# Kernel tuning notes

Hardware: AMD Instinct MI355X
Metric: run time of the kernel (lower is better)

Reference implementation:

```python
import jax, jax.numpy as jnp
import numpy as np

BN_EPS = 1e-5


def _bn_relu(h, gamma, beta):
    # BatchNorm1d in training mode: batch stats over the edge dimension, biased var
    mu = jnp.mean(h, axis=0)
    var = jnp.mean((h - mu) ** 2, axis=0)
    return jax.nn.relu((h - mu) * jax.lax.rsqrt(var + BN_EPS) * gamma + beta)


def setup_inputs() -> dict:
    key = jax.random.key(0)
    ks = jax.random.split(key, 6)
    B, P, C, O, K = 8, 2048, 64, 64, 20  # clouds, points/cloud, in_ch, out_ch, knn
    N = B * P
    x = jax.random.normal(ks[0], (N, C), jnp.float32)
    pos = jax.random.normal(ks[1], (N, 3), jnp.float32)
    batch = jnp.repeat(jnp.arange(B, dtype=jnp.int32), P)  # sorted cloud ids
    # MLP params: Linear(2C, O) -> BN -> ReLU -> Linear(O, O) -> BN -> ReLU
    W1 = jax.random.normal(ks[2], (O, 2 * C), jnp.float32) / np.sqrt(2 * C)
    b1 = jnp.zeros((O,), jnp.float32)
    g1 = jnp.ones((O,), jnp.float32)
    beta1 = jnp.zeros((O,), jnp.float32)
    W2 = jax.random.normal(ks[3], (O, O), jnp.float32) / np.sqrt(O)
    b2 = jnp.zeros((O,), jnp.float32)
    g2 = jnp.ones((O,), jnp.float32)
    beta2 = jnp.zeros((O,), jnp.float32)
    return {"x": x, "pos": pos, "batch": batch, "W1": W1, "b1": b1, "g1": g1,
            "beta1": beta1, "W2": W2, "b2": b2, "g2": g2, "beta2": beta2, "k": K}


def reference(x, pos, batch, W1, b1, g1, beta1, W2, b2, g2, beta2, k):
    N, C = x.shape
    B = int(batch[-1]) + 1          # equal-size, sorted clouds
    P = N // B
    p = pos.reshape(B, P, -1)
    # knn_graph (loop=False): brute-force squared distances per cloud
    sq = jnp.sum(p * p, axis=-1)                      # [B,P]
    d2 = sq[:, :, None] + sq[:, None, :] - 2.0 * jnp.einsum('bpd,bqd->bpq', p, p)
    d2 = jnp.where(jnp.eye(P, dtype=bool)[None], jnp.inf, d2)  # no self-loops
    _, nbr = jax.lax.top_k(-d2, k)                    # [B,P,k] neighbor idx in cloud
    offset = (jnp.arange(B, dtype=nbr.dtype) * P)[:, None, None]
    # torch_cluster knn_graph flow='source_to_target': row = neighbor j, col = center i
    row = (nbr + offset).reshape(-1)                  # [N*k]
    col = jnp.repeat(jnp.arange(N, dtype=row.dtype), k)
    x_r = x[row]
    edge_features = jnp.concatenate([x_r, x[col] - x_r], axis=1)  # [N*k, 2C]
    h = _bn_relu(edge_features @ W1.T + b1, g1, beta1)
    h = _bn_relu(h @ W2.T + b2, g2, beta2)
    out = jax.ops.segment_max(h, row, num_segments=N)
    # torch_scatter scatter(reduce='max') leaves empty rows at 0
    return jnp.where(jnp.isneginf(out), 0.0, out)
```

## Files before the change

### kernel.cpp

```cpp
#include <hip/hip_runtime.h>

constexpr int BATCH = 8;
constexpr int PPC   = 2048;
constexpr int NPT   = BATCH * PPC;
constexpr int OCH   = 64;
constexpr int KNN_K = 20;
constexpr int NEDGE = NPT * KNN_K;
constexpr int REVCAP = 128;
constexpr int OVCAP  = 8192;
constexpr int QCAP   = 48;

typedef short short8 __attribute__((ext_vector_type(8)));
typedef float float4v __attribute__((ext_vector_type(4)));

__device__ __forceinline__ int xcd_swizzle(int b, int nper) {
  return (b & 7) * nper + (b >> 3);
}

__device__ __forceinline__ unsigned short bfr(float f) {
  unsigned u = __float_as_uint(f);
  return (unsigned short)((u + 0x7FFFu + ((u >> 16) & 1u)) >> 16);
}
__device__ __forceinline__ short8 pack8(float4 a, float4 b) {
  short8 r;
  r[0] = (short)bfr(a.x); r[1] = (short)bfr(a.y);
  r[2] = (short)bfr(a.z); r[3] = (short)bfr(a.w);
  r[4] = (short)bfr(b.x); r[5] = (short)bfr(b.y);
  r[6] = (short)bfr(b.z); r[7] = (short)bfr(b.w);
  return r;
}
__device__ __forceinline__ unsigned umed3(unsigned a, unsigned b, unsigned c) {
  unsigned d;
  asm("v_med3_u32 %0, %1, %2, %3" : "=v"(d) : "v"(a), "v"(b), "v"(c));
  return d;
}

__global__ __launch_bounds__(256) void knn_kernel(const float* __restrict__ pos,
                                                  int* __restrict__ nbr,
                                                  int* __restrict__ cnt,
                                                  int* __restrict__ ovf_cnt,
                                                  int* __restrict__ ovf,
                                                  int* __restrict__ rev) {
  __shared__ float4 cps[8 * 257];
  __shared__ unsigned long long qk[16][QCAP];
  __shared__ int qn[16];
  const int t  = threadIdx.x;
  const int pl = t >> 4;
  const int s  = t & 15;
  const int lane = t & 63;
  const int eb = xcd_swizzle(blockIdx.x, NPT / 16 / 8);
  const int i  = eb * 16 + pl;
  const int cbase = i & ~(PPC - 1);

  for (int u = t; u < PPC; u += 256) {
    int j = cbase + u;
    float ax = pos[3 * j], ay = pos[3 * j + 1], az = pos[3 * j + 2];
    cps[(u >> 8) * 257 + (u & 255)] = make_float4(ax, ay, az, ax * ax + ay * ay + az * az);
  }
  if (t < 16) qn[t] = 0;
  __syncthreads();

  const int il = i - cbase;
  const float4 me = cps[(il >> 8) * 257 + (il & 255)];
  const float px = me.x, py = me.y, pz = me.z, sqi = me.w;
  const int jbase = s * 128;
  const float4* __restrict__ cp = &cps[(s >> 1) * 257 + (s & 1) * 128];

  unsigned kd[3];
  kd[0] = kd[1] = kd[2] = 0xFFFFFFFFu;
  for (int u = 0; u < 128; ++u) {
    float4 c = cp[u];
    float d2 = sqi + c.w - 2.0f * (px * c.x + py * c.y + pz * c.z);
    d2 = d2 > 0.f ? d2 : 0.f;
    unsigned ck = __float_as_uint(d2);
    ck = (jbase + u == il) ? 0xFFFFFFFFu : ck;
    kd[2] = umed3(kd[1], kd[2], ck);
    kd[1] = umed3(kd[0], kd[1], ck);
    kd[0] = kd[0] < ck ? kd[0] : ck;
  }

  unsigned T = 0xFFFFFFFFu;
  int cum = 0;
  const int grp = lane & 48;
#pragma unroll
  for (int r = 0; r < KNN_K; ++r) {
    unsigned w = kd[0];
#pragma unroll
    for (int m = 1; m < 16; m <<= 1) {
      unsigned o = (unsigned)__shfl_xor((int)w, m, 16);
      w = o < w ? o : w;
    }
    bool pop = (kd[0] == w);
    unsigned long long bal = __ballot(pop);
    int mcount = __popc((int)((bal >> grp) & 0xFFFFull));
    if (cum < KNN_K) T = w;
    cum += mcount;
    if (pop) { kd[0] = kd[1]; kd[1] = kd[2]; kd[2] = 0xFFFFFFFFu; }
  }

  for (int u = 0; u < 128; ++u) {
    float4 c = cp[u];
    float d2 = sqi + c.w - 2.0f * (px * c.x + py * c.y + pz * c.z);
    d2 = d2 > 0.f ? d2 : 0.f;
    unsigned ck = __float_as_uint(d2);
    ck = (jbase + u == il) ? 0xFFFFFFFFu : ck;
    if (ck <= T) {
      int slot = atomicAdd(&qn[pl], 1);
      if (slot < QCAP)
        qk[pl][slot] = ((unsigned long long)ck << 32) | (unsigned)(jbase + u);
    }
  }
  __syncthreads();

  int n = qn[pl]; n = n < QCAP ? n : QCAP;
  for (int base = 0; base < n; base += 16) {
    int e = base + s;
    if (e < n) {
      unsigned long long mk = qk[pl][e];
      int rank = 0;
      for (int o = 0; o < n; ++o) rank += (qk[pl][o] < mk) ? 1 : 0;
      if (rank < KNN_K) {
        int j = cbase + (int)(mk & 0xFFFFFFFFull);
        int eid = i * KNN_K + rank;
        nbr[eid] = j;
        int slot = atomicAdd(&cnt[j], 1);
        if (slot < REVCAP) rev[j * REVCAP + slot] = i;
        else { int ov = atomicAdd(ovf_cnt, 1); if (ov < OVCAP) ovf[ov] = eid; }
      }
    }
  }
}

__global__ __launch_bounds__(256) void node_gemm(const float* __restrict__ x,
                                                 const float* __restrict__ W1,
                                                 float* __restrict__ yv,
                                                 float* __restrict__ zv) {
  __shared__ float wa[64][65];
  __shared__ float wb[64][65];
  __shared__ float xs[4][64];
  const int t = threadIdx.x;
  for (int m = t; m < 8192; m += 256) {
    int o = m >> 7, c2 = m & 127;
    float w = W1[m];
    if (c2 < 64) wa[c2][o] = w; else wb[c2 - 64][o] = w;
  }
  const int nl = t >> 6, o = t & 63;
  xs[nl][o] = x[(size_t)(blockIdx.x * 4 + nl) * 64 + o];
  __syncthreads();
  float accA = 0.f, accB = 0.f;
#pragma unroll 8
  for (int c = 0; c < 64; ++c) {
    float xv = xs[nl][c];
    accA = fmaf(xv, wa[c][o], accA);
    accB = fmaf(xv, wb[c][o], accB);
  }
  size_t n = (size_t)blockIdx.x * 4 + nl;
  yv[n * 64 + o] = accA - accB;
  zv[n * 64 + o] = accB;
}

__global__ __launch_bounds__(256) void bn1_stats(const int* __restrict__ nbr,
                                                 const float4* __restrict__ yv4,
                                                 const float4* __restrict__ zv4,
                                                 const float* __restrict__ b1,
                                                 float* __restrict__ stats) {
  const int t  = threadIdx.x;
  const int c4 = t & 15;
  const int lane = t & 63;
  const int eb = xcd_swizzle(blockIdx.x, NPT / 16 / 8);
  const int i  = eb * 16 + (t >> 4);
  const float4 bo = reinterpret_cast<const float4*>(b1)[c4];
  float4 z = zv4[(size_t)i * 16 + c4];
  float4 zb = make_float4(z.x + bo.x, z.y + bo.y, z.z + bo.z, z.w + bo.w);
  int jA = nbr[i * KNN_K + c4];
  int jB = nbr[i * KNN_K + 16 + (c4 & 3)];
  float4 s1 = make_float4(0, 0, 0, 0), s2 = make_float4(0, 0, 0, 0);
#pragma unroll
  for (int q = 0; q < 16; ++q) {
    int j = __shfl(jA, (lane & 48) + q);
    float4 y = yv4[(size_t)j * 16 + c4];
    float sx = y.x + zb.x, sy = y.y + zb.y, sz = y.z + zb.z, sw = y.w + zb.w;
    s1.x += sx; s1.y += sy; s1.z += sz; s1.w += sw;
    s2.x += sx * sx; s2.y += sy * sy; s2.z += sz * sz; s2.w += sw * sw;
  }
#pragma unroll
  for (int q = 0; q < 4; ++q) {
    int j = __shfl(jB, (lane & 48) + q);
    float4 y = yv4[(size_t)j * 16 + c4];
    float sx = y.x + zb.x, sy = y.y + zb.y, sz = y.z + zb.z, sw = y.w + zb.w;
    s1.x += sx; s1.y += sy; s1.z += sz; s1.w += sw;
    s2.x += sx * sx; s2.y += sy * sy; s2.z += sz * sz; s2.w += sw * sw;
  }
  s1.x += __shfl_xor(s1.x, 16); s1.y += __shfl_xor(s1.y, 16);
  s1.z += __shfl_xor(s1.z, 16); s1.w += __shfl_xor(s1.w, 16);
  s2.x += __shfl_xor(s2.x, 16); s2.y += __shfl_xor(s2.y, 16);
  s2.z += __shfl_xor(s2.z, 16); s2.w += __shfl_xor(s2.w, 16);
  s1.x += __shfl_xor(s1.x, 32); s1.y += __shfl_xor(s1.y, 32);
  s1.z += __shfl_xor(s1.z, 32); s1.w += __shfl_xor(s1.w, 32);
  s2.x += __shfl_xor(s2.x, 32); s2.y += __shfl_xor(s2.y, 32);
  s2.z += __shfl_xor(s2.z, 32); s2.w += __shfl_xor(s2.w, 32);
  __shared__ float ss[2][64];
  if (t < 128) { ss[0][t & 63] = 0.f; }
  __syncthreads();
  if ((t & 48) == 0) {
    atomicAdd(&ss[0][c4 * 4 + 0], s1.x); atomicAdd(&ss[0][c4 * 4 + 1], s1.y);
    atomicAdd(&ss[0][c4 * 4 + 2], s1.z); atomicAdd(&ss[0][c4 * 4 + 3], s1.w);
    atomicAdd(&ss[1][c4 * 4 + 0], s2.x); atomicAdd(&ss[1][c4 * 4 + 1], s2.y);
    atomicAdd(&ss[1][c4 * 4 + 2], s2.z); atomicAdd(&ss[1][c4 * 4 + 3], s2.w);
  }
  __syncthreads();
  if (t < 64)       atomicAdd(&stats[t], ss[0][t]);
  else if (t < 128) atomicAdd(&stats[64 + (t - 64)], ss[1][t - 64]);
}

__global__ __launch_bounds__(256) void scale_yz(
    const float4* __restrict__ yv4, const float4* __restrict__ zv4,
    const float* __restrict__ stats1, const float* __restrict__ g1,
    const float* __restrict__ beta1, const float* __restrict__ b1,
    float4* __restrict__ ys4, float4* __restrict__ zs4) {
  const int idx = blockIdx.x * 256 + threadIdx.x;
  const int c4 = idx & 15;
  constexpr float invE = 1.0f / NEDGE;
  float a[4], c[4];
#pragma unroll
  for (int q = 0; q < 4; ++q) {
    int ch = c4 * 4 + q;
    float mu  = stats1[ch] * invE;
    float var = stats1[64 + ch] * invE - mu * mu;
    float av  = g1[ch] * rsqrtf(var + 1e-5f);
    a[q] = av;
    c[q] = fmaf(b1[ch], av, beta1[ch] - mu * av);
  }
  float4 y = yv4[idx];
  float4 z = zv4[idx];
  ys4[idx] = make_float4(y.x * a[0], y.y * a[1], y.z * a[2], y.w * a[3]);
  zs4[idx] = make_float4(fmaf(z.x, a[0], c[0]), fmaf(z.y, a[1], c[1]),
                         fmaf(z.z, a[2], c[2]), fmaf(z.w, a[3], c[3]));
}

__global__ __launch_bounds__(256) void gemm2_row(
    const float4* __restrict__ ys4, const float4* __restrict__ zs4,
    const float* __restrict__ W2, const float* __restrict__ b2,
    const int* __restrict__ cnt, const int* __restrict__ rev,
    float* __restrict__ stats2, float* __restrict__ mmax,
    float* __restrict__ mmin) {
  __shared__ float ss[2][64];
  const int t = threadIdx.x, lane = t & 63;
  const int col = lane & 15, quad = lane >> 4;
  const int eb = xcd_swizzle(blockIdx.x, NPT / 16 / 8);
  const int wid = eb * 4 + (t >> 6);

  short8 bf0[4], bf1[4];
  const float4* __restrict__ W2v = (const float4*)W2;
#pragma unroll
  for (int nt = 0; nt < 4; ++nt) {
    int row = nt * 16 + col;
    float4 wa = W2v[row * 16 + quad * 2];
    float4 wb = W2v[row * 16 + quad * 2 + 1];
    float4 wc = W2v[row * 16 + 8 + quad * 2];
    float4 wd = W2v[row * 16 + 8 + quad * 2 + 1];
    bf0[nt] = pack8(wa, wb);
    bf1[nt] = pack8(wc, wd);
  }
  float b2r[4];
#pragma unroll
  for (int nt = 0; nt < 4; ++nt) b2r[nt] = b2[nt * 16 + col];

  float s1[4] = {0, 0, 0, 0}, s2[4] = {0, 0, 0, 0};
  for (int rr = 0; rr < 4; ++rr) {
    const int row = wid * 4 + rr;
    int n = cnt[row]; n = n < REVCAP ? n : REVCAP;
    int rv0 = (lane < n) ? rev[(size_t)row * REVCAP + lane] : 0;
    int rv1 = (64 + lane < n) ? rev[(size_t)row * REVCAP + 64 + lane] : 0;
    float4 ya = ys4[(size_t)row * 16 + quad * 2];
    float4 yb = ys4[(size_t)row * 16 + quad * 2 + 1];
    float4 yc = ys4[(size_t)row * 16 + 8 + quad * 2];
    float4 yd = ys4[(size_t)row * 16 + 8 + quad * 2 + 1];
    float mx[4], mn[4];
#pragma unroll
    for (int nt = 0; nt < 4; ++nt) { mx[nt] = -1e30f; mn[nt] = 1e30f; }

    auto tile_body = [&](int tbase, float4 za, float4 zb, float4 zc, float4 zd) {
      float h[16];
      h[0]  = ya.x + za.x; h[1]  = ya.y + za.y; h[2]  = ya.z + za.z; h[3]  = ya.w + za.w;
      h[4]  = yb.x + zb.x; h[5]  = yb.y + zb.y; h[6]  = yb.z + zb.z; h[7]  = yb.w + zb.w;
      h[8]  = yc.x + zc.x; h[9]  = yc.y + zc.y; h[10] = yc.z + zc.z; h[11] = yc.w + zc.w;
      h[12] = yd.x + zd.x; h[13] = yd.y + zd.y; h[14] = yd.z + zd.z; h[15] = yd.w + zd.w;
      short8 af0, af1;
#pragma unroll
      for (int q = 0; q < 8; ++q) {
        float u0 = h[q]     > 0.f ? h[q]     : 0.f;
        float u1 = h[8 + q] > 0.f ? h[8 + q] : 0.f;
        af0[q] = (short)bfr(u0);
        af1[q] = (short)bfr(u1);
      }
      float4v acc[4];
#pragma unroll
      for (int nt = 0; nt < 4; ++nt) {
        acc[nt] = (float4v){0.f, 0.f, 0.f, 0.f};
        acc[nt] = __builtin_amdgcn_mfma_f32_16x16x32_bf16(af0, bf0[nt], acc[nt], 0, 0, 0);
        acc[nt] = __builtin_amdgcn_mfma_f32_16x16x32_bf16(af1, bf1[nt], acc[nt], 0, 0, 0);
      }
#pragma unroll
      for (int r = 0; r < 4; ++r) {
        bool v = (tbase + quad * 4 + r) < n;
#pragma unroll
        for (int nt = 0; nt < 4; ++nt) {
          float val = acc[nt][r] + b2r[nt];
          if (v) {
            s1[nt] += val; s2[nt] += val * val;
            mx[nt] = val > mx[nt] ? val : mx[nt];
            mn[nt] = val < mn[nt] ? val : mn[nt];
          }
        }
      }
    };

    int icA = __shfl(rv0, col);       icA = (col < n) ? icA : 0;
    int icB = __shfl(rv0, 16 + col);  icB = (16 + col < n) ? icB : 0;
    float4 zAa = zs4[(size_t)icA * 16 + quad * 2];
    float4 zAb = zs4[(size_t)icA * 16 + quad * 2 + 1];
    float4 zAc = zs4[(size_t)icA * 16 + 8 + quad * 2];
    float4 zAd = zs4[(size_t)icA * 16 + 8 + quad * 2 + 1];
    float4 zBa = zs4[(size_t)icB * 16 + quad * 2];
    float4 zBb = zs4[(size_t)icB * 16 + quad * 2 + 1];
    float4 zBc = zs4[(size_t)icB * 16 + 8 + quad * 2];
    float4 zBd = zs4[(size_t)icB * 16 + 8 + quad * 2 + 1];
    tile_body(0, zAa, zAb, zAc, zAd);
    if (n > 16) tile_body(16, zBa, zBb, zBc, zBd);
    for (int ti = 2; ti * 16 < n; ++ti) {
      int gi = ti * 16 + col;
      int v0 = __shfl(rv0, gi & 63);
      int v1 = __shfl(rv1, gi & 63);
      int ic = (gi < 64) ? v0 : v1;
      ic = (gi < n) ? ic : 0;
      float4 za = zs4[(size_t)ic * 16 + quad * 2];
      float4 zb = zs4[(size_t)ic * 16 + quad * 2 + 1];
      float4 zc = zs4[(size_t)ic * 16 + 8 + quad * 2];
      float4 zd = zs4[(size_t)ic * 16 + 8 + quad * 2 + 1];
      tile_body(ti * 16, za, zb, zc, zd);
    }
#pragma unroll
    for (int nt = 0; nt < 4; ++nt) {
      mx[nt] = fmaxf(mx[nt], __shfl_xor(mx[nt], 16));
      mx[nt] = fmaxf(mx[nt], __shfl_xor(mx[nt], 32));
      mn[nt] = fminf(mn[nt], __shfl_xor(mn[nt], 16));
      mn[nt] = fminf(mn[nt], __shfl_xor(mn[nt], 32));
    }
    if (quad == 0) {
#pragma unroll
      for (int nt = 0; nt < 4; ++nt) {
        mmax[(size_t)row * 64 + nt * 16 + col] = mx[nt];
        mmin[(size_t)row * 64 + nt * 16 + col] = mn[nt];
      }
    }
  }
  if (t < 128) ss[t >> 6][t & 63] = 0.f;
  __syncthreads();
#pragma unroll
  for (int nt = 0; nt < 4; ++nt) {
    s1[nt] += __shfl_xor(s1[nt], 16);
    s1[nt] += __shfl_xor(s1[nt], 32);
    s2[nt] += __shfl_xor(s2[nt], 16);
    s2[nt] += __shfl_xor(s2[nt], 32);
  }
  if (quad == 0) {
#pragma unroll
    for (int nt = 0; nt < 4; ++nt) {
      atomicAdd(&ss[0][nt * 16 + col], s1[nt]);
      atomicAdd(&ss[1][nt * 16 + col], s2[nt]);
    }
  }
  __syncthreads();
  if (t < 64)       atomicAdd(&stats2[t], ss[0][t]);
  else if (t < 128) atomicAdd(&stats2[64 + (t - 64)], ss[1][t - 64]);
}

__global__ __launch_bounds__(256) void finalize_out(
    const float* __restrict__ stats2, const float* __restrict__ g2,
    const float* __restrict__ beta2, const int* __restrict__ cnt,
    const float* __restrict__ mmax, const float* __restrict__ mmin,
    const int* __restrict__ ovf_cnt, const int* __restrict__ ovf,
    const int* __restrict__ nbr, const float* __restrict__ ys,
    const float* __restrict__ zs, const float* __restrict__ W2,
    const float* __restrict__ b2, float* __restrict__ outp) {
  const int idx = blockIdx.x * 256 + threadIdx.x;
  const int row = idx >> 6, ch = idx & 63;
  constexpr float invE = 1.0f / NEDGE;
  float mu  = stats2[ch] * invE;
  float var = stats2[64 + ch] * invE - mu * mu;
  float a2  = g2[ch] * rsqrtf(var + 1e-5f);
  float c2  = beta2[ch] - mu * a2;
  float h = (a2 >= 0.f) ? mmax[idx] : mmin[idx];
  int ov = ovf_cnt[0]; ov = ov > OVCAP ? OVCAP : ov;
  for (int u = 0; u < ov; ++u) {
    int e = ovf[u];
    if (nbr[e] == row) {
      int ic = e / KNN_K;
      float accv = 0.f;
      for (int k = 0; k < 64; ++k) {
        float hh = ys[(size_t)row * 64 + k] + zs[(size_t)ic * 64 + k];
        hh = hh > 0.f ? hh : 0.f;
        accv = fmaf(hh, W2[ch * 64 + k], accv);
      }
      float v = accv + b2[ch];
      if (a2 >= 0.f) h = v > h ? v : h; else h = v < h ? v : h;
    }
  }
  float o = (cnt[row] > 0) ? fmaf(h, a2, c2) : 0.0f;
  outp[idx] = o > 0.f ? o : 0.f;
}

extern "C" void kernel_launch(void* const* d_in, const int* in_sizes, int n_in,
                              void* d_out, int out_size, void* d_ws, size_t ws_size,
                              hipStream_t stream) {
  (void)in_sizes; (void)n_in; (void)out_size; (void)ws_size;
  const float* x     = (const float*)d_in[0];
  const float* pos   = (const float*)d_in[1];
  const float* W1    = (const float*)d_in[3];
  const float* b1    = (const float*)d_in[4];
  const float* g1    = (const float*)d_in[5];
  const float* beta1 = (const float*)d_in[6];
  const float* W2    = (const float*)d_in[7];
  const float* b2    = (const float*)d_in[8];
  const float* g2    = (const float*)d_in[9];
  const float* beta2 = (const float*)d_in[10];
  float* outp = (float*)d_out;

  char* w = (char*)d_ws;
  int*   nbr     = (int*)w;
  float* yv      = (float*)(w + 1310720);
  float* zv      = (float*)(w + 5505024);
  float* stats   = (float*)(w + 9699328);
  int*   cnt     = (int*)(w + 9700352);
  int*   ovf_cnt = (int*)(w + 9765888);
  int*   ovf     = (int*)(w + 9765952);
  int*   rev     = (int*)(w + 9798720);
  float* mmax    = (float*)(w + 18187328);
  float* mmin    = (float*)(w + 22381632);
  float* ys      = (float*)(w + 26575936);
  float* zs      = (float*)(w + 30770240);

  hipMemsetAsync(stats, 0, 1024, stream);
  hipMemsetAsync(cnt, 0, 65536 + 64, stream);

  knn_kernel<<<NPT / 16, 256, 0, stream>>>(pos, nbr, cnt, ovf_cnt, ovf, rev);
  node_gemm<<<NPT / 4, 256, 0, stream>>>(x, W1, yv, zv);
  bn1_stats<<<NPT / 16, 256, 0, stream>>>(nbr, (const float4*)yv, (const float4*)zv, b1, stats);
  scale_yz<<<NPT * 16 / 256, 256, 0, stream>>>(
      (const float4*)yv, (const float4*)zv, stats, g1, beta1, b1,
      (float4*)ys, (float4*)zs);
  gemm2_row<<<NPT / 16, 256, 0, stream>>>(
      (const float4*)ys, (const float4*)zs, W2, b2,
      cnt, rev, stats + 128, mmax, mmin);
  finalize_out<<<NPT * 64 / 256, 256, 0, stream>>>(
      stats + 128, g2, beta2, cnt, mmax, mmin, ovf_cnt, ovf, nbr,
      ys, zs, W2, b2, outp);
}
```

Baseline: 231.5 us.

## Cheapen kNN distance key, batch node GEMM rows, prefetch rows in gemm2

The kNN scan now ranks candidates with a reduced key, 1000 + 0.5|c|^2 - p·c, built from fused FMAs. The offset keeps the key positive so its bit pattern sorts like the float. The full squared distance is computed only for candidates that pass a slightly widened threshold, which protects the exact ordering but may queue a few more entries. node_gemm processes 16 nodes per block with register accumulators, reusing each weight load across 4 nodes. gemm2_row loads its four row counts in one go and prefetches the next row's reverse indices and ys values, overlapping memory latency with compute; it also reads the rev entries without the bounds guard.

```diff
diff --git a/kernel.cpp b/kernel.cpp
--- a/kernel.cpp
+++ b/kernel.cpp
@@ -70,9 +70,8 @@
   kd[0] = kd[1] = kd[2] = 0xFFFFFFFFu;
   for (int u = 0; u < 128; ++u) {
     float4 c = cp[u];
-    float d2 = sqi + c.w - 2.0f * (px * c.x + py * c.y + pz * c.z);
-    d2 = d2 > 0.f ? d2 : 0.f;
-    unsigned ck = __float_as_uint(d2);
+    float pr = fmaf(-px, c.x, fmaf(-py, c.y, fmaf(-pz, c.z, fmaf(0.5f, c.w, 1000.f))));
+    unsigned ck = __float_as_uint(pr);
     ck = (jbase + u == il) ? 0xFFFFFFFFu : ck;
     kd[2] = umed3(kd[1], kd[2], ck);
     kd[1] = umed3(kd[0], kd[1], ck);
@@ -97,17 +96,19 @@
     cum += mcount;
     if (pop) { kd[0] = kd[1]; kd[1] = kd[2]; kd[2] = 0xFFFFFFFFu; }
   }
+  const unsigned Tq = T + 16;
 
   for (int u = 0; u < 128; ++u) {
     float4 c = cp[u];
-    float d2 = sqi + c.w - 2.0f * (px * c.x + py * c.y + pz * c.z);
-    d2 = d2 > 0.f ? d2 : 0.f;
-    unsigned ck = __float_as_uint(d2);
+    float pr = fmaf(-px, c.x, fmaf(-py, c.y, fmaf(-pz, c.z, fmaf(0.5f, c.w, 1000.f))));
+    unsigned ck = __float_as_uint(pr);
     ck = (jbase + u == il) ? 0xFFFFFFFFu : ck;
-    if (ck <= T) {
+    if (ck <= Tq) {
+      float d2 = sqi + c.w - 2.0f * (px * c.x + py * c.y + pz * c.z);
+      d2 = d2 > 0.f ? d2 : 0.f;
       int slot = atomicAdd(&qn[pl], 1);
       if (slot < QCAP)
-        qk[pl][slot] = ((unsigned long long)ck << 32) | (unsigned)(jbase + u);
+        qk[pl][slot] = ((unsigned long long)__float_as_uint(d2) << 32) | (unsigned)(jbase + u);
     }
   }
   __syncthreads();
@@ -137,26 +138,34 @@
                                                  float* __restrict__ zv) {
   __shared__ float wa[64][65];
   __shared__ float wb[64][65];
-  __shared__ float xs[4][64];
+  __shared__ float xs[16][64];
   const int t = threadIdx.x;
   for (int m = t; m < 8192; m += 256) {
     int o = m >> 7, c2 = m & 127;
     float w = W1[m];
     if (c2 < 64) wa[c2][o] = w; else wb[c2 - 64][o] = w;
   }
-  const int nl = t >> 6, o = t & 63;
-  xs[nl][o] = x[(size_t)(blockIdx.x * 4 + nl) * 64 + o];
-  __syncthreads();
-  float accA = 0.f, accB = 0.f;
-#pragma unroll 8
+  for (int m = t; m < 1024; m += 256)
+    xs[m >> 6][m & 63] = x[(size_t)blockIdx.x * 1024 + m];
+  __syncthreads();
+  const int g = t >> 6, o = t & 63;
+  float accA[4] = {0, 0, 0, 0}, accB[4] = {0, 0, 0, 0};
+#pragma unroll 4
   for (int c = 0; c < 64; ++c) {
-    float xv = xs[nl][c];
-    accA = fmaf(xv, wa[c][o], accA);
-    accB = fmaf(xv, wb[c][o], accB);
-  }
-  size_t n = (size_t)blockIdx.x * 4 + nl;
-  yv[n * 64 + o] = accA - accB;
-  zv[n * 64 + o] = accB;
+    float w_a = wa[c][o], w_b = wb[c][o];
+#pragma unroll
+    for (int q = 0; q < 4; ++q) {
+      float xv = xs[g * 4 + q][c];
+      accA[q] = fmaf(xv, w_a, accA[q]);
+      accB[q] = fmaf(xv, w_b, accB[q]);
+    }
+  }
+#pragma unroll
+  for (int q = 0; q < 4; ++q) {
+    size_t n = (size_t)blockIdx.x * 16 + g * 4 + q;
+    yv[n * 64 + o] = accA[q] - accB[q];
+    zv[n * 64 + o] = accB[q];
+  }
 }
 
 __global__ __launch_bounds__(256) void bn1_stats(const int* __restrict__ nbr,
@@ -266,16 +275,34 @@
 #pragma unroll
   for (int nt = 0; nt < 4; ++nt) b2r[nt] = b2[nt * 16 + col];
 
+  int4 cq = *reinterpret_cast<const int4*>(&cnt[wid * 4]);
+  int nA[4] = {cq.x, cq.y, cq.z, cq.w};
+#pragma unroll
+  for (int q = 0; q < 4; ++q) nA[q] = nA[q] < REVCAP ? nA[q] : REVCAP;
+
   float s1[4] = {0, 0, 0, 0}, s2[4] = {0, 0, 0, 0};
+  int rv0 = rev[(size_t)(wid * 4) * REVCAP + lane];
+  int rv1 = rev[(size_t)(wid * 4) * REVCAP + 64 + lane];
+  float4 ya = ys4[(size_t)(wid * 4) * 16 + quad * 2];
+  float4 yb = ys4[(size_t)(wid * 4) * 16 + quad * 2 + 1];
+  float4 yc = ys4[(size_t)(wid * 4) * 16 + 8 + quad * 2];
+  float4 yd = ys4[(size_t)(wid * 4) * 16 + 8 + quad * 2 + 1];
+
+#pragma unroll
   for (int rr = 0; rr < 4; ++rr) {
     const int row = wid * 4 + rr;
-    int n = cnt[row]; n = n < REVCAP ? n : REVCAP;
-    int rv0 = (lane < n) ? rev[(size_t)row * REVCAP + lane] : 0;
-    int rv1 = (64 + lane < n) ? rev[(size_t)row * REVCAP + 64 + lane] : 0;
-    float4 ya = ys4[(size_t)row * 16 + quad * 2];
-    float4 yb = ys4[(size_t)row * 16 + quad * 2 + 1];
-    float4 yc = ys4[(size_t)row * 16 + 8 + quad * 2];
-    float4 yd = ys4[(size_t)row * 16 + 8 + quad * 2 + 1];
+    const int n = nA[rr];
+    int nrv0 = 0, nrv1 = 0;
+    float4 nya, nyb, nyc, nyd;
+    if (rr < 3) {
+      const int nrow = row + 1;
+      nrv0 = rev[(size_t)nrow * REVCAP + lane];
+      nrv1 = rev[(size_t)nrow * REVCAP + 64 + lane];
+      nya = ys4[(size_t)nrow * 16 + quad * 2];
+      nyb = ys4[(size_t)nrow * 16 + quad * 2 + 1];
+      nyc = ys4[(size_t)nrow * 16 + 8 + quad * 2];
+      nyd = ys4[(size_t)nrow * 16 + 8 + quad * 2 + 1];
+    }
     float mx[4], mn[4];
 #pragma unroll
     for (int nt = 0; nt < 4; ++nt) { mx[nt] = -1e30f; mn[nt] = 1e30f; }
@@ -354,6 +381,8 @@
         mmin[(size_t)row * 64 + nt * 16 + col] = mn[nt];
       }
     }
+    rv0 = nrv0; rv1 = nrv1;
+    ya = nya; yb = nyb; yc = nyc; yd = nyd;
   }
   if (t < 128) ss[t >> 6][t & 63] = 0.f;
   __syncthreads();
@@ -445,7 +474,7 @@
   hipMemsetAsync(cnt, 0, 65536 + 64, stream);
 
   knn_kernel<<<NPT / 16, 256, 0, stream>>>(pos, nbr, cnt, ovf_cnt, ovf, rev);
-  node_gemm<<<NPT / 4, 256, 0, stream>>>(x, W1, yv, zv);
+  node_gemm<<<NPT / 16, 256, 0, stream>>>(x, W1, yv, zv);
   bn1_stats<<<NPT / 16, 256, 0, stream>>>(nbr, (const float4*)yv, (const float4*)zv, b1, stats);
   scale_yz<<<NPT * 16 / 256, 256, 0, stream>>>(
       (const float4*)yv, (const float4*)zv, stats, g1, beta1, b1,
```

Result: faster. 215.3 us (-7.0%).
